# Kernel optimization log

Hardware: AMD Instinct MI355X
Metric: run time of the kernel (lower is better)

The kernel has to match this reference:

```python
import jax, jax.numpy as jnp
import numpy as np

N_HEAD = 16
ROPE_BASE = 10000.0


def _rope_tables(T, head_dim, dtype=jnp.float32):
    inv_freq = 1.0 / (ROPE_BASE ** (jnp.arange(0, head_dim, 2, dtype=jnp.float32) / head_dim))
    t = jnp.arange(T, dtype=jnp.float32)
    freqs = t[:, None] * inv_freq[None, :]          # [T, D/2]
    emb = jnp.concatenate([freqs, freqs], axis=-1)  # [T, D]
    return jnp.cos(emb).astype(dtype), jnp.sin(emb).astype(dtype)


def _rotate_half(x):
    d = x.shape[-1] // 2
    return jnp.concatenate([-x[..., d:], x[..., :d]], axis=-1)


def setup_inputs() -> dict:
    key = jax.random.key(0)
    ks = jax.random.split(key, 5)
    B, T, C = 2, 2048, 2048
    s = 1.0 / np.sqrt(C)
    return {
        "x": jax.random.normal(ks[0], (B, T, C), dtype=jnp.float32),
        "wq": jax.random.normal(ks[1], (C, C), dtype=jnp.float32) * s,
        "wk": jax.random.normal(ks[2], (C, C), dtype=jnp.float32) * s,
        "wv": jax.random.normal(ks[3], (C, C), dtype=jnp.float32) * s,
        "wo": jax.random.normal(ks[4], (C, C), dtype=jnp.float32) * s,
    }


def reference(x, wq, wk, wv, wo):
    B, T, C = x.shape
    H = N_HEAD
    D = C // H

    def heads(y):  # [B,T,C] -> [B,H,T,D]
        return y.reshape(B, T, H, D).transpose(0, 2, 1, 3)

    q = heads(x @ wq)
    k = heads(x @ wk)
    v = heads(x @ wv)

    cos, sin = _rope_tables(T, D, x.dtype)          # [T, D]
    cos = cos[None, None, :, :]
    sin = sin[None, None, :, :]
    q = q * cos + _rotate_half(q) * sin
    k = k * cos + _rotate_half(k) * sin

    scale = 1.0 / np.sqrt(D)
    scores = jnp.einsum('bhqd,bhkd->bhqk', q, k) * scale   # [B,H,T,T]
    causal = jnp.tril(jnp.ones((T, T), dtype=bool))
    scores = jnp.where(causal[None, None, :, :], scores, jnp.finfo(scores.dtype).min)
    attn = jax.nn.softmax(scores, axis=-1)
    y = jnp.einsum('bhqk,bhkd->bhqd', attn, v)             # [B,H,T,D]
    y = y.transpose(0, 2, 1, 3).reshape(B, T, C)
    return y @ wo
```

## Files before the change

kernel.cpp:

```cpp
#include <hip/hip_runtime.h>
#include <hip/hip_bf16.h>
#include <math.h>


#define TT 2048
#define CCn 2048
#define HH 16
#define DD 128
#define MMr 4096
#define NQKV 6144

typedef __attribute__((ext_vector_type(8))) short s16x8;
typedef __attribute__((ext_vector_type(4))) short s16x4;
typedef __attribute__((ext_vector_type(4))) float f32x4;

__device__ __forceinline__ short bf16_of(float f) {
  unsigned u = __float_as_uint(f);
  unsigned r = u + 0x7fffu + ((u >> 16) & 1u);
  return (short)(r >> 16);
}
__device__ __forceinline__ float f_of_bf16(short s) {
  return __uint_as_float(((unsigned)(unsigned short)s) << 16);
}
__device__ __forceinline__ float ex2(float x) { return exp2f(x); }

__device__ __forceinline__ void lds_load16(const void* g, void* l) {
  __builtin_amdgcn_global_load_lds((__attribute__((address_space(1))) void*)g,
                                   (__attribute__((address_space(3))) void*)l,
                                   16, 0, 0);
}

__global__ __launch_bounds__(256) void k_tables(float* __restrict__ cosT,
                                                float* __restrict__ sinT) {
  int idx = blockIdx.x * 256 + threadIdx.x;
  int t = idx >> 6, i = idx & 63;
  float inv = powf(10000.0f, -(float)i * (1.0f / 64.0f));
  float f = (float)t * inv;
  cosT[idx] = cosf(f);
  sinT[idx] = sinf(f);
}

__global__ __launch_bounds__(256) void k_cast_x(const float* __restrict__ x,
                                                short* __restrict__ xb) {
  int i = blockIdx.x * 256 + threadIdx.x;
  f32x4 v = ((const f32x4*)x)[i];
  s16x4 o;
#pragma unroll
  for (int j = 0; j < 4; ++j) o[j] = bf16_of(v[j]);
  ((s16x4*)xb)[i] = o;
}

__global__ __launch_bounds__(256) void k_wtrans4(const float* __restrict__ w0,
                                                 const float* __restrict__ w1,
                                                 const float* __restrict__ w2,
                                                 const float* __restrict__ w3,
                                                 short* __restrict__ wqkvT,
                                                 short* __restrict__ woT) {
  __shared__ float tile[32][33];
  int z = blockIdx.z;
  const float* w = (z == 0) ? w0 : (z == 1) ? w1 : (z == 2) ? w2 : w3;
  short* wt = (z == 3) ? woT : wqkvT + (size_t)z * 2048 * 2048;
  int n0 = blockIdx.x * 32, k0 = blockIdx.y * 32;
  int tx = threadIdx.x & 31, ty = threadIdx.x >> 5;
#pragma unroll
  for (int j = 0; j < 4; ++j) {
    int k = ty * 4 + j;
    tile[k][tx] = w[(size_t)(k0 + k) * CCn + n0 + tx];
  }
  __syncthreads();
#pragma unroll
  for (int j = 0; j < 4; ++j) {
    int n = ty * 4 + j;
    wt[(size_t)(n0 + n) * CCn + k0 + tx] = bf16_of(tile[tx][n]);
  }
}

__global__ __launch_bounds__(256) void k_vtrans(const short* __restrict__ src,
                                                short* __restrict__ dst) {
  __shared__ short tile[32][33];
  int bh = blockIdx.y, b = bh >> 4, h = bh & 15;
  int dt = blockIdx.x & 3, tt = blockIdx.x >> 2;
  int tx = threadIdx.x & 31, ty = threadIdx.x >> 5;
  const short* sp = src + ((size_t)(b * TT + tt * 32)) * NQKV + 4096 + h * DD + dt * 32;
#pragma unroll
  for (int j = 0; j < 4; ++j) {
    int tr = ty * 4 + j;
    tile[tr][tx] = sp[(size_t)tr * NQKV + tx];
  }
  __syncthreads();
  short* dp = dst + ((size_t)(bh * DD + dt * 32)) * TT + tt * 32;
#pragma unroll
  for (int j = 0; j < 4; ++j) {
    int dr = ty * 4 + j;
    dp[(size_t)dr * TT + tx] = tile[tx][dr];
  }
}

__global__ __launch_bounds__(256) void k_rope2(const short* __restrict__ qkv,
                                               const float* __restrict__ cosT,
                                               const float* __restrict__ sinT,
                                               short* __restrict__ Qb,
                                               short* __restrict__ Kb, float kmul) {
  int which = blockIdx.y;
  int coff = which << 11;
  short* dstb = which ? Kb : Qb;
  float mul = which ? kmul : 1.0f;
  int idx = blockIdx.x * 256 + threadIdx.x;
  int i4 = (idx & 15) * 4;
  int h = (idx >> 4) & 15;
  int t = (idx >> 8) & 2047;
  int b = idx >> 19;
  const short* row = qkv + ((size_t)(b * TT + t)) * NQKV + coff + h * DD;
  s16x4 v0 = *(const s16x4*)(row + i4);
  s16x4 v1 = *(const s16x4*)(row + i4 + 64);
  f32x4 c4 = *(const f32x4*)(cosT + t * 64 + i4);
  f32x4 s4 = *(const f32x4*)(sinT + t * 64 + i4);
  s16x4 o0, o1;
#pragma unroll
  for (int j = 0; j < 4; ++j) {
    float a = f_of_bf16(v0[j]), bb = f_of_bf16(v1[j]);
    o0[j] = bf16_of((a * c4[j] - bb * s4[j]) * mul);
    o1[j] = bf16_of((bb * c4[j] + a * s4[j]) * mul);
  }
  short* orow = dstb + ((size_t)((b * HH + h) * TT + t)) * DD;
  *(s16x4*)(orow + i4) = o0;
  *(s16x4*)(orow + i4 + 64) = o1;
}

template <int WNF, bool BF16OUT>
__global__ __launch_bounds__(512) void k_g8(const short* __restrict__ A,
                                            const short* __restrict__ Bt,
                                            void* __restrict__ Cout,
                                            int M, int N, int K) {
  constexpr int BN = WNF * 64;
  constexpr int AHS = 128 * 32;
  constexpr int BHS = BN * 32;
  constexpr int NBL = BN / 128;
  constexpr int WNH = WNF / 2;
  __shared__ short smem[4 * AHS + 4 * BHS];
  const int tid = threadIdx.x, wid = tid >> 6, lane = tid & 63;
  const int wm = wid >> 2, wn = wid & 3;
  const int lr = lane & 15, lk = lane >> 4;
  const int swz = (lk ^ ((lr >> 1) & 3)) * 8;

  int nwg = gridDim.x, orig = blockIdx.x;
  int xcd = orig & 7, bidx = orig >> 3;
  int q = nwg >> 3, rmd = nwg & 7;
  int wg = (xcd < rmd) ? (xcd * (q + 1) + bidx)
                       : (rmd * (q + 1) + (xcd - rmd) * q + bidx);
  const int NBM = M >> 7;
  const int m0 = (wg % NBM) * 128, n0 = (wg / NBM) * BN;

  auto stageA = [&](int buf, int ks, int kt) {
    int row = tid >> 2;
    int cc = (tid & 3) ^ ((row >> 1) & 3);
    lds_load16(A + (size_t)(m0 + row) * K + kt * 64 + ks * 32 + cc * 8,
               smem + buf * 2 * AHS + ks * AHS + tid * 8);
  };
  auto stageB = [&](int buf, int ks, int kt) {
#pragma unroll
    for (int l = 0; l < NBL; ++l) {
      int lin = l * 512 + tid;
      int row = lin >> 2;
      int cc = (lin & 3) ^ ((row >> 1) & 3);
      lds_load16(Bt + (size_t)(n0 + row) * K + kt * 64 + ks * 32 + cc * 8,
                 smem + 4 * AHS + buf * 2 * BHS + ks * BHS + lin * 8);
    }
  };

  s16x8 af[4], bfr[WNH];
  f32x4 acc[4][WNF] = {};

#define LDA(BUF, KS)                                                           \
  _Pragma("unroll") for (int i = 0; i < 4; ++i) af[i] =                        \
      *(const s16x8*)(smem + (BUF) * 2 * AHS + (KS) * AHS +                    \
                      (wm * 64 + i * 16 + lr) * 32 + swz);
#define LDB(BUF, KS, NH)                                                       \
  _Pragma("unroll") for (int j = 0; j < WNH; ++j) bfr[j] =                     \
      *(const s16x8*)(smem + 4 * AHS + (BUF) * 2 * BHS + (KS) * BHS +          \
                      (wn * (WNF * 16) + ((NH) * WNH + j) * 16 + lr) * 32 +    \
                      swz);
#define BAR_MFMA(NH)                                                           \
  __builtin_amdgcn_s_barrier();                                                \
  asm volatile("s_waitcnt lgkmcnt(0)" ::: "memory");                           \
  __builtin_amdgcn_s_setprio(1);                                               \
  _Pragma("unroll") for (int i = 0; i < 4; ++i)                                \
      _Pragma("unroll") for (int j = 0; j < WNH; ++j)                          \
      acc[i][(NH) * WNH + j] = __builtin_amdgcn_mfma_f32_16x16x32_bf16(        \
          af[i], bfr[j], acc[i][(NH) * WNH + j], 0, 0, 0);                     \
  __builtin_amdgcn_s_setprio(0);
#define VMW(cond, NN)                                                          \
  if (cond) { asm volatile("s_waitcnt vmcnt(%0)" ::"i"(NN) : "memory"); }      \
  else      { asm volatile("s_waitcnt vmcnt(0)" ::: "memory"); }

  const int nk = K >> 6, niter = nk >> 1;
  stageA(0, 0, 0); stageB(0, 0, 0);
  stageA(0, 1, 0); stageB(0, 1, 0);
  stageA(1, 0, 1); stageB(1, 0, 1);
  asm volatile("s_waitcnt vmcnt(%0)" ::"i"(1 + NBL) : "memory");
  __builtin_amdgcn_s_barrier();

#pragma unroll 1
  for (int it = 0; it < niter; ++it) {
    const int kt1 = 2 * it + 1, kt2 = 2 * it + 2, kt3 = 2 * it + 3;
    const bool s2 = kt2 < nk, s3 = kt3 < nk;
    LDA(0, 0); LDB(0, 0, 0);
    stageA(1, 1, kt1); stageB(1, 1, kt1);
    BAR_MFMA(0);
    __builtin_amdgcn_s_barrier();
    LDB(0, 0, 1);
    if (s2) stageA(0, 0, kt2);
    BAR_MFMA(1);
    __builtin_amdgcn_s_barrier();
    LDA(0, 1); LDB(0, 1, 0);
    if (s2) stageB(0, 0, kt2);
    BAR_MFMA(0);
    __builtin_amdgcn_s_barrier();
    LDB(0, 1, 1);
    if (s2) stageA(0, 1, kt2);
    BAR_MFMA(1);
    VMW(s2, 2 + NBL);
    __builtin_amdgcn_s_barrier();
    LDA(1, 0); LDB(1, 0, 0);
    if (s2) stageB(0, 1, kt2);
    BAR_MFMA(0);
    __builtin_amdgcn_s_barrier();
    LDB(1, 0, 1);
    if (s3) stageA(1, 0, kt3);
    BAR_MFMA(1);
    __builtin_amdgcn_s_barrier();
    LDA(1, 1); LDB(1, 1, 0);
    if (s3) stageB(1, 0, kt3);
    BAR_MFMA(0);
    __builtin_amdgcn_s_barrier();
    LDB(1, 1, 1);
    BAR_MFMA(1);
    VMW(s3, 1 + NBL);
    __builtin_amdgcn_s_barrier();
  }
#undef LDA
#undef LDB
#undef BAR_MFMA
#undef VMW

#pragma unroll
  for (int i = 0; i < 4; ++i)
#pragma unroll
    for (int j = 0; j < WNF; ++j) {
      int row0 = m0 + wm * 64 + i * 16 + lk * 4;
      int col = n0 + wn * (WNF * 16) + j * 16 + lr;
#pragma unroll
      for (int rr = 0; rr < 4; ++rr) {
        if (BF16OUT)
          ((short*)Cout)[(size_t)(row0 + rr) * N + col] = bf16_of(acc[i][j][rr]);
        else
          ((float*)Cout)[(size_t)(row0 + rr) * N + col] = acc[i][j][rr];
      }
    }
}

__global__ __launch_bounds__(512) void k_attn(const short* __restrict__ Qb,
                                              const short* __restrict__ Kb,
                                              const short* __restrict__ Vt,
                                              short* __restrict__ yb) {
  __shared__ short Ks[2][64 * 128];
  __shared__ short Vs[128 * 64];
  __shared__ short Ps[8][16 * 72];
  const int tid = threadIdx.x, wid = tid >> 6, lane = tid & 63;
  const int lr = lane & 15, lk = lane >> 4;
  const int bh = blockIdx.y, bx = blockIdx.x;
  const size_t baseQK = (size_t)bh * TT * DD;
  const int b = bh >> 4, h = bh & 15;

  auto stageK = [&](int bi, int kt2) {
#pragma unroll
    for (int it = 0; it < 2; ++it) {
      int ch = it * 512 + tid;
      int r = ch >> 4, cc = ch & 15;
      int cs = cc ^ (r & 7);
      lds_load16(Kb + baseQK + (size_t)(kt2 * 64 + r) * DD + cs * 8,
                 &Ks[bi][(size_t)(it * 512 + wid * 64) * 8]);
    }
  };
  auto stageV = [&](int kt2) {
#pragma unroll
    for (int it = 0; it < 2; ++it) {
      int ch = it * 512 + tid;
      int d = ch >> 3, kc = ch & 7;
      int cs = kc ^ (d & 7);
      lds_load16(Vt + baseQK + (size_t)d * TT + kt2 * 64 + cs * 8,
                 &Vs[(size_t)(it * 512 + wid * 64) * 8]);
    }
  };

#pragma unroll 1
  for (int pass = 0; pass < 2; ++pass) {
    const int qt = pass ? (15 - bx) : bx;
    const int q0 = qt * 128;
    const int qg = q0 + wid * 16 + lr;
    s16x8 qf[4];
#pragma unroll
    for (int ds = 0; ds < 4; ++ds)
      qf[ds] = *(const s16x8*)(Qb + baseQK + (size_t)qg * DD + (ds * 4 + lk) * 8);

    float mrun = -3.0e38f, lrun = 0.f;
    f32x4 yacc[8] = {};

    const int nkt = 2 * qt + 2;
    stageK(0, 0);
    stageV(0);
    __syncthreads();
    int buf = 0;
#pragma unroll 1
    for (int kt = 0; kt < nkt; ++kt) {
      if (kt + 1 < nkt) stageK(buf ^ 1, kt + 1);
      f32x4 sf[4] = {};
#pragma unroll
      for (int sub = 0; sub < 4; ++sub) {
        int kr = sub * 16 + lr;
#pragma unroll
        for (int ds = 0; ds < 4; ++ds) {
          int cc = (ds * 4 + lk) ^ (kr & 7);
          s16x8 kf = *(const s16x8*)(&Ks[buf][kr * 128 + cc * 8]);
          sf[sub] = __builtin_amdgcn_mfma_f32_16x16x32_bf16(kf, qf[ds], sf[sub], 0, 0, 0);
        }
      }
      const int kvbase = kt * 64;
      if (kvbase + 63 > q0 + wid * 16) {
#pragma unroll
        for (int sub = 0; sub < 4; ++sub)
#pragma unroll
          for (int r = 0; r < 4; ++r) {
            int kv = kvbase + sub * 16 + lk * 4 + r;
            if (kv > qg) sf[sub][r] = -3.0e38f;
          }
      }
      float tmax = -3.0e38f;
#pragma unroll
      for (int sub = 0; sub < 4; ++sub)
#pragma unroll
        for (int r = 0; r < 4; ++r) tmax = fmaxf(tmax, sf[sub][r]);
      tmax = fmaxf(tmax, __shfl_xor(tmax, 16, 64));
      tmax = fmaxf(tmax, __shfl_xor(tmax, 32, 64));
      if (!__all(tmax <= mrun + 11.0f)) {
        float mnew = fmaxf(mrun, tmax);
        float alpha = ex2(mrun - mnew);
        mrun = mnew;
        lrun *= alpha;
        float ar[4];
#pragma unroll
        for (int r = 0; r < 4; ++r) ar[r] = __shfl(alpha, lk * 4 + r, 64);
#pragma unroll
        for (int dn = 0; dn < 8; ++dn)
#pragma unroll
          for (int r = 0; r < 4; ++r) yacc[dn][r] *= ar[r];
      }
      float psum = 0.f;
#pragma unroll
      for (int sub = 0; sub < 4; ++sub) {
        s16x4 pq;
#pragma unroll
        for (int r = 0; r < 4; ++r) {
          float p = ex2(sf[sub][r] - mrun);
          psum += p;
          pq[r] = bf16_of(p);
        }
        *(s16x4*)(&Ps[wid][lr * 72 + sub * 16 + lk * 4]) = pq;
      }
      psum += __shfl_xor(psum, 16, 64);
      psum += __shfl_xor(psum, 32, 64);
      lrun += psum;
      __syncthreads();
      s16x8 pf0 = *(const s16x8*)(&Ps[wid][lr * 72 + lk * 8]);
      s16x8 pf1 = *(const s16x8*)(&Ps[wid][lr * 72 + 32 + lk * 8]);
#pragma unroll
      for (int dn = 0; dn < 8; ++dn) {
        int d = dn * 16 + lr;
        s16x8 vf0 = *(const s16x8*)(&Vs[d * 64 + (lk ^ (d & 7)) * 8]);
        yacc[dn] = __builtin_amdgcn_mfma_f32_16x16x32_bf16(pf0, vf0, yacc[dn], 0, 0, 0);
        s16x8 vf1 = *(const s16x8*)(&Vs[d * 64 + ((4 + lk) ^ (d & 7)) * 8]);
        yacc[dn] = __builtin_amdgcn_mfma_f32_16x16x32_bf16(pf1, vf1, yacc[dn], 0, 0, 0);
      }
      __syncthreads();
      if (kt + 1 < nkt) stageV(kt + 1);
      buf ^= 1;
    }
    float linv = 1.f / lrun;
    float lr4[4];
#pragma unroll
    for (int r = 0; r < 4; ++r) lr4[r] = __shfl(linv, lk * 4 + r, 64);
#pragma unroll
    for (int dn = 0; dn < 8; ++dn)
#pragma unroll
      for (int r = 0; r < 4; ++r) {
        int t = q0 + wid * 16 + lk * 4 + r;
        int c = h * DD + dn * 16 + lr;
        yb[((size_t)(b * TT + t)) * CCn + c] = bf16_of(yacc[dn][r] * lr4[r]);
      }
  }
}

extern "C" void kernel_launch(void* const* d_in, const int* in_sizes, int n_in,
                              void* d_out, int out_size, void* d_ws, size_t ws_size,
                              hipStream_t stream) {
  const float* x = (const float*)d_in[0];
  const float* wq = (const float*)d_in[1];
  const float* wk = (const float*)d_in[2];
  const float* wv = (const float*)d_in[3];
  const float* wo = (const float*)d_in[4];
  float* out = (float*)d_out;
  char* ws = (char*)d_ws;

  short* xb = (short*)(ws + 0);
  short* wqkvT = (short*)(ws + 16777216);
  short* woT = (short*)(ws + 41943040);
  short* qkv = (short*)(ws + 50331648);
  short* yb = (short*)(ws + 50331648);
  short* Qb = (short*)(ws + 100663296);
  short* Kb = (short*)(ws + 117440512);
  short* Vt = (short*)(ws + 134217728);
  float* cosT = (float*)(ws + 150994944);
  float* sinT = (float*)(ws + 151519232);

  const float kmul = 1.4426950408889634f / sqrtf(128.0f);

  k_tables<<<512, 256, 0, stream>>>(cosT, sinT);
  k_cast_x<<<8192, 256, 0, stream>>>(x, xb);
  k_wtrans4<<<dim3(64, 64, 4), 256, 0, stream>>>(wq, wk, wv, wo, wqkvT, woT);

  k_g8<6, true><<<512, 512, 0, stream>>>(xb, wqkvT, qkv, MMr, NQKV, CCn);

  k_rope2<<<dim3(4096, 2), 256, 0, stream>>>(qkv, cosT, sinT, Qb, Kb, kmul);
  k_vtrans<<<dim3(256, 32), 256, 0, stream>>>(qkv, Vt);

  k_attn<<<dim3(8, 32), 512, 0, stream>>>(Qb, Kb, Vt, yb);

  k_g8<4, false><<<256, 512, 0, stream>>>(yb, woT, out, MMr, CCn, CCn);
}
```

Measured before the change: 399.4 us.

## Triple-buffer K/V tiles in attention with explicit vmcnt waits

Converts the attention kernel's K (double-buffered) and V (single-buffered) LDS staging into a three-deep ring for both K and V. Tiles are prefetched two iterations ahead, and completion is gated by manual s_waitcnt vmcnt counts plus raw s_barrier calls instead of __syncthreads. The barrier between the P write and the PV MMA is dropped because each wave reads only its own Ps slice. The V swizzle also gains an extra XOR bit to reduce LDS bank conflicts. In exchange, LDS use rises (which may reduce occupancy), and correctness depends on the hand-counted vmcnt values matching the number of outstanding loads.

```diff
diff --git a/kernel.cpp b/kernel.cpp
--- a/kernel.cpp
+++ b/kernel.cpp
@@ -263,8 +263,8 @@
                                               const short* __restrict__ Kb,
                                               const short* __restrict__ Vt,
                                               short* __restrict__ yb) {
-  __shared__ short Ks[2][64 * 128];
-  __shared__ short Vs[128 * 64];
+  __shared__ short Ks[3][64 * 128];
+  __shared__ short Vs[3][128 * 64];
   __shared__ short Ps[8][16 * 72];
   const int tid = threadIdx.x, wid = tid >> 6, lane = tid & 63;
   const int lr = lane & 15, lk = lane >> 4;
@@ -279,17 +279,17 @@
       int r = ch >> 4, cc = ch & 15;
       int cs = cc ^ (r & 7);
       lds_load16(Kb + baseQK + (size_t)(kt2 * 64 + r) * DD + cs * 8,
-                 &Ks[bi][(size_t)(it * 512 + wid * 64) * 8]);
+                 &Ks[bi][(size_t)(it * 512 + (tid & ~63)) * 8]);
     }
   };
-  auto stageV = [&](int kt2) {
+  auto stageV = [&](int bi, int kt2) {
 #pragma unroll
     for (int it = 0; it < 2; ++it) {
       int ch = it * 512 + tid;
       int d = ch >> 3, kc = ch & 7;
-      int cs = kc ^ (d & 7);
+      int cs = kc ^ ((d & 7) ^ ((d >> 3) & 1));
       lds_load16(Vt + baseQK + (size_t)d * TT + kt2 * 64 + cs * 8,
-                 &Vs[(size_t)(it * 512 + wid * 64) * 8]);
+                 &Vs[bi][(size_t)(it * 512 + (tid & ~63)) * 8]);
     }
   };
 
@@ -307,13 +307,19 @@
     f32x4 yacc[8] = {};
 
     const int nkt = 2 * qt + 2;
-    stageK(0, 0);
-    stageV(0);
-    __syncthreads();
-    int buf = 0;
+    stageK(0, 0); stageV(0, 0);
+    stageK(1, 1); stageV(1, 1);
+    if (nkt > 2) {
+      stageK(2, 2); stageV(2, 2);
+      asm volatile("s_waitcnt vmcnt(8)" ::: "memory");
+    } else {
+      asm volatile("s_waitcnt vmcnt(4)" ::: "memory");
+    }
+    __builtin_amdgcn_s_barrier();
+
 #pragma unroll 1
     for (int kt = 0; kt < nkt; ++kt) {
-      if (kt + 1 < nkt) stageK(buf ^ 1, kt + 1);
+      const int buf = kt - (kt / 3) * 3;
       f32x4 sf[4] = {};
 #pragma unroll
       for (int sub = 0; sub < 4; ++sub) {
@@ -370,20 +376,27 @@
       psum += __shfl_xor(psum, 16, 64);
       psum += __shfl_xor(psum, 32, 64);
       lrun += psum;
-      __syncthreads();
       s16x8 pf0 = *(const s16x8*)(&Ps[wid][lr * 72 + lk * 8]);
       s16x8 pf1 = *(const s16x8*)(&Ps[wid][lr * 72 + 32 + lk * 8]);
 #pragma unroll
       for (int dn = 0; dn < 8; ++dn) {
         int d = dn * 16 + lr;
-        s16x8 vf0 = *(const s16x8*)(&Vs[d * 64 + (lk ^ (d & 7)) * 8]);
+        int g = (d & 7) ^ ((d >> 3) & 1);
+        s16x8 vf0 = *(const s16x8*)(&Vs[buf][d * 64 + (lk ^ g) * 8]);
         yacc[dn] = __builtin_amdgcn_mfma_f32_16x16x32_bf16(pf0, vf0, yacc[dn], 0, 0, 0);
-        s16x8 vf1 = *(const s16x8*)(&Vs[d * 64 + ((4 + lk) ^ (d & 7)) * 8]);
+        s16x8 vf1 = *(const s16x8*)(&Vs[buf][d * 64 + ((4 + lk) ^ g) * 8]);
         yacc[dn] = __builtin_amdgcn_mfma_f32_16x16x32_bf16(pf1, vf1, yacc[dn], 0, 0, 0);
       }
-      __syncthreads();
-      if (kt + 1 < nkt) stageV(kt + 1);
-      buf ^= 1;
+      __builtin_amdgcn_s_barrier();
+      if (kt + 3 < nkt) {
+        stageK(buf, kt + 3); stageV(buf, kt + 3);
+        asm volatile("s_waitcnt vmcnt(8)" ::: "memory");
+      } else if (kt + 3 == nkt) {
+        asm volatile("s_waitcnt vmcnt(4)" ::: "memory");
+      } else {
+        asm volatile("s_waitcnt vmcnt(0)" ::: "memory");
+      }
+      __builtin_amdgcn_s_barrier();
     }
     float linv = 1.f / lrun;
     float lr4[4];
```

Result: no change. 401.8 us (+0.6%).
